# Kernel optimization log

Measured on AMD Instinct MI355X. Metric: run time of the kernel, lower is better.

## Reference

```python
import jax, jax.numpy as jnp
import numpy as np

B, T, D = 2, 1024, 1024
NH, HD = 16, 64          # attention heads, head dim (D = NH*HD)
M = 16                   # LRU block size
H = D // M               # number of LRU blocks = 64
EPS = 1e-5
ROPE_BASE = 10000.0


def rmsnorm(x, w):
    ms = jnp.mean(x * x, axis=-1, keepdims=True)
    return x * jax.lax.rsqrt(ms + EPS) * w


def rope_tables(t_len, dtype):
    inv_freq = 1.0 / (ROPE_BASE ** (jnp.arange(0, HD, 2, dtype=jnp.float32) / HD))
    freqs = jnp.arange(t_len, dtype=jnp.float32)[:, None] * inv_freq[None, :]  # [T, HD/2]
    emb = jnp.concatenate([freqs, freqs], axis=-1)                              # [T, HD]
    return emb.astype(dtype)


def apply_rope(x, emb):
    # x: [B, T, NH, HD]
    cos = jnp.cos(emb)[None, :, None, :]
    sin = jnp.sin(emb)[None, :, None, :]
    x1, x2 = jnp.split(x, 2, axis=-1)
    return x * cos + jnp.concatenate([-x2, x1], axis=-1) * sin


def setup_inputs() -> dict:
    key = jax.random.key(0)
    ks = jax.random.split(key, 7)
    w = lambda k, shape: jax.random.normal(k, shape, dtype=jnp.float32) * 0.02
    return {
        "x": jax.random.normal(ks[0], (B, T, D), dtype=jnp.float32),
        "attn_norm_w": jnp.ones((D,), jnp.float32),
        "w_qkv": w(ks[1], (D, 3 * D)),
        "w_attn_out": w(ks[2], (D, D)),
        "lru_norm_w": jnp.ones((D,), jnp.float32),
        "w_v": w(ks[3], (D, D)),
        "w_a": w(ks[4], (D, H * M * (M + 1))),
        "w_out_proj": w(ks[5], (D, D)),
    }


def reference(x, attn_norm_w, w_qkv, w_attn_out, lru_norm_w, w_v, w_a, w_out_proj):
    # ---- RoPE causal attention block (residual) ----
    h = rmsnorm(x, attn_norm_w)
    qkv = (h @ w_qkv).reshape(B, T, 3, NH, HD)
    q, k, v = qkv[:, :, 0], qkv[:, :, 1], qkv[:, :, 2]
    emb = rope_tables(T, x.dtype)
    q = apply_rope(q, emb)
    k = apply_rope(k, emb)
    scores = jnp.einsum("bthd,bshd->bhts", q, k) / jnp.sqrt(jnp.asarray(HD, x.dtype))
    causal = jnp.tril(jnp.ones((T, T), dtype=bool))
    scores = jnp.where(causal[None, None], scores, jnp.asarray(-1e30, x.dtype))
    attn = jax.nn.softmax(scores, axis=-1)
    o = jnp.einsum("bhts,bshd->bthd", attn, v).reshape(B, T, D)
    x = x + o @ w_attn_out

    # ---- BlockDiagonalLRU block (residual) ----
    h2 = rmsnorm(x, lru_norm_w)
    vv = (h2 @ w_v).reshape(B, T, H, M)
    gates = jax.nn.softmax((h2 @ w_a).reshape(B, T, H, M, M + 1), axis=-1)
    a0 = gates[..., 0]   # [B, T, H, M]
    A = gates[..., 1:]   # [B, T, H, M, M]

    def step(state, inp):
        A_t, a0_t, v_t = inp  # [B,H,M,M], [B,H,M], [B,H,M]
        new = jnp.einsum("bhij,bhj->bhi", A_t, state) + a0_t * v_t
        return new, new

    init = jnp.zeros((B, H, M), x.dtype)
    _, outs = jax.lax.scan(
        step, init,
        (jnp.moveaxis(A, 1, 0), jnp.moveaxis(a0, 1, 0), jnp.moveaxis(vv, 1, 0)),
    )
    h_out = jnp.moveaxis(outs, 0, 1).reshape(B, T, D)
    return x + h_out @ w_out_proj
```

## Files before the change

kernel.cpp:

```cpp
#include <hip/hip_runtime.h>


typedef unsigned short u16;
typedef unsigned int   u32;
typedef __bf16 bf16x8 __attribute__((ext_vector_type(8)));
typedef float  f32x4  __attribute__((ext_vector_type(4)));

#define B_  2
#define T_  1024
#define D_  1024
#define NH_ 16
#define HD_ 64
#define H_  64
#define M_  16

__device__ __forceinline__ float b2f(u16 u) {
    return __uint_as_float(((u32)u) << 16);
}
__device__ __forceinline__ u16 f2b(float f) {
    u32 u = __float_as_uint(f);
    u32 r = (u + 0x7FFFu + ((u >> 16) & 1u)) >> 16;
    return (u16)r;
}
__device__ __forceinline__ float blo(u32 u) { return __uint_as_float(u << 16); }
__device__ __forceinline__ float bhi(u32 u) { return __uint_as_float(u & 0xFFFF0000u); }

__device__ __forceinline__ void stage16(const void* gp, void* lp) {
    typedef __attribute__((address_space(1))) const unsigned int GU;
    typedef __attribute__((address_space(3))) unsigned int LU;
    __builtin_amdgcn_global_load_lds((GU*)gp, (LU*)lp, 16, 0, 0);
}

template<int BM, int BN, int BK, int MODE, bool TRUNCK, bool CAUSAL, int SWZ>
__global__ __launch_bounds__(256) void gemm_bt(
    const u16* __restrict__ A, const u16* __restrict__ Bt,
    void* __restrict__ Cout, void* __restrict__ Cout2, void* __restrict__ Cout3,
    const float* __restrict__ addend,
    int M, int N, int K, long strideA, long strideB, long strideC)
{
    constexpr int MT = BM / 32;
    constexpr int NT = BN / 32;
    constexpr int KCH = BK / 8;
    const int z  = blockIdx.z;
    int bx = blockIdx.x, by = blockIdx.y;
    if (SWZ == 2) {
        int f = by * gridDim.x + bx;
        int xcd = f & 7, k = f >> 3;
        by = k & 15;
        bx = xcd * (gridDim.x >> 3) + (k >> 4);
    }
    const int m0 = by * BM;
    const int n0 = bx * BN;
    if (CAUSAL && n0 > m0 + BM - 1) return;
    const int Keff = TRUNCK ? (K < m0 + BM ? K : m0 + BM) : K;

    const u16* Ab = A  + (size_t)z * (size_t)strideA;
    const u16* Bb = Bt + (size_t)z * (size_t)strideB;

    __shared__ alignas(16) u16 As[BM * BK];
    __shared__ alignas(16) u16 Bs[BN * BK];

    const int tid  = threadIdx.x;
    const int lane = tid & 63, w = tid >> 6;
    const int wr = w >> 1, wc = w & 1;
    const int quad = lane >> 4, l16 = lane & 15;

    f32x4 acc[MT][NT] = {};

    constexpr int AITER = (BM * BK / 8) / 256;
    constexpr int BITER = (BN * BK / 8) / 256;

    for (int k0 = 0; k0 < Keff; k0 += BK) {
        #pragma unroll
        for (int it = 0; it < AITER; ++it) {
            int c = it * 256 + tid;
            int m = c / KCH, kc = c % KCH;
            stage16(Ab + (size_t)(m0 + m) * K + k0 + kc * 8,
                    &As[(it * 256 + w * 64) * 8]);
        }
        #pragma unroll
        for (int it = 0; it < BITER; ++it) {
            int c = it * 256 + tid;
            int n = c / KCH, kc = c % KCH;
            stage16(Bb + (size_t)(n0 + n) * K + k0 + kc * 8,
                    &Bs[(it * 256 + w * 64) * 8]);
        }
        __syncthreads();

        #pragma unroll
        for (int kk = 0; kk < BK; kk += 32) {
            bf16x8 af[MT], bfr[NT];
            #pragma unroll
            for (int mt = 0; mt < MT; ++mt)
                af[mt] = *(const bf16x8*)&As[(wr * (BM / 2) + mt * 16 + l16) * BK + kk + quad * 8];
            #pragma unroll
            for (int nt = 0; nt < NT; ++nt)
                bfr[nt] = *(const bf16x8*)&Bs[(wc * (BN / 2) + nt * 16 + l16) * BK + kk + quad * 8];
            #pragma unroll
            for (int mt = 0; mt < MT; ++mt)
                #pragma unroll
                for (int nt = 0; nt < NT; ++nt)
                    acc[mt][nt] = __builtin_amdgcn_mfma_f32_16x16x32_bf16(
                        af[mt], bfr[nt], acc[mt][nt], 0, 0, 0);
        }
        __syncthreads();
    }

    if (MODE == 6) {
        const int reg = n0 >> 10;
        const int hh  = ((n0 & 1023) >> 6) + wc;
        #pragma unroll
        for (int mt = 0; mt < MT; ++mt) {
            #pragma unroll
            for (int r = 0; r < 4; ++r) {
                int row = m0 + wr * (BM / 2) + mt * 16 + quad * 4 + r;
                int t = row & (T_ - 1), bb = row >> 10;
                size_t obase = ((size_t)(bb * NH_ + hh) * T_ + t) * HD_;
                if (reg == 2) {
                    #pragma unroll
                    for (int nt = 0; nt < 4; ++nt)
                        ((u16*)Cout3)[obase + nt * 16 + l16] = f2b(acc[mt][nt][r]);
                } else {
                    u16* dst = (reg == 0) ? (u16*)Cout : (u16*)Cout2;
                    #pragma unroll
                    for (int nt = 0; nt < 2; ++nt) {
                        int i = nt * 16 + l16;
                        float ang = (float)t * exp2f(-(float)i * 0.41524101186092034f);
                        float sn, cs;
                        sincosf(ang, &sn, &cs);
                        float q1 = acc[mt][nt][r], q2 = acc[mt][nt + 2][r];
                        dst[obase + i]      = f2b(q1 * cs - q2 * sn);
                        dst[obase + i + 32] = f2b(q2 * cs + q1 * sn);
                    }
                }
            }
        }
        return;
    }
    #pragma unroll
    for (int mt = 0; mt < MT; ++mt) {
        #pragma unroll
        for (int nt = 0; nt < NT; ++nt) {
            #pragma unroll
            for (int r = 0; r < 4; ++r) {
                int row = m0 + wr * (BM / 2) + mt * 16 + quad * 4 + r;
                int col = n0 + wc * (BN / 2) + nt * 16 + l16;
                float val = acc[mt][nt][r];
                if (MODE == 0) {
                    if (addend) val += addend[(size_t)row * N + col];
                    ((float*)Cout)[(size_t)z * (size_t)strideC + (size_t)row * N + col] = val;
                } else if (MODE == 1) {
                    ((u16*)Cout)[(size_t)z * (size_t)strideC + (size_t)row * N + col] = f2b(val);
                } else if (MODE == 2) {
                    size_t idx = ((size_t)(z >> 4) * T_ + row) * (size_t)D_ + (z & 15) * HD_ + col;
                    ((u16*)Cout)[idx] = f2b(val);
                } else {
                    const int t  = row & (T_ - 1);
                    const int bb = m0 >> 10;
                    const int cg = (n0 >> 4) + wc * (BN / 32) + nt;
                    if (cg >= 1088) {
                        const int hh = cg - 1088;
                        ((float*)Cout2)[(((size_t)(bb * 64 + hh)) * T_ + t) * 16 + l16] = val;
                    } else {
                        const int hh  = cg / 17;
                        const int rem = cg - hh * 17;
                        ((u16*)Cout)[(((size_t)(bb * 64 + hh)) * T_ + t) * 272 + rem * 16 + l16] = f2b(val);
                    }
                }
            }
        }
    }
}

__global__ __launch_bounds__(256) void rmsnorm_k(
    const float* __restrict__ x, const float* __restrict__ w, u16* __restrict__ out)
{
    const int row = blockIdx.x, tid = threadIdx.x;
    float4 v = ((const float4*)(x + (size_t)row * D_))[tid];
    float ss = v.x * v.x + v.y * v.y + v.z * v.z + v.w * v.w;
    #pragma unroll
    for (int o = 32; o >= 1; o >>= 1) ss += __shfl_xor(ss, o, 64);
    __shared__ float red[4];
    if ((tid & 63) == 0) red[tid >> 6] = ss;
    __syncthreads();
    ss = red[0] + red[1] + red[2] + red[3];
    float scale = rsqrtf(ss * (1.0f / D_) + 1e-5f);
    float4 wv = ((const float4*)w)[tid];
    ushort4 o4;
    o4.x = f2b(v.x * scale * wv.x);
    o4.y = f2b(v.y * scale * wv.y);
    o4.z = f2b(v.z * scale * wv.z);
    o4.w = f2b(v.w * scale * wv.w);
    ((ushort4*)(out + (size_t)row * D_))[tid] = o4;
}

__global__ void convT_all(
    const float* __restrict__ wqkv, const float* __restrict__ wao,
    const float* __restrict__ wv,   const float* __restrict__ wa,
    const float* __restrict__ wop,
    u16* __restrict__ wqkvT, u16* __restrict__ waoT,
    u16* __restrict__ waT,   u16* __restrict__ wopT)
{
    const int x = blockIdx.x;
    const float* in; u16* out; int C, xb;
    if (x < 96)       { in = wqkv; out = wqkvT; C = 3072;  xb = x; }
    else if (x < 128) { in = wao;  out = waoT;  C = 1024;  xb = x - 96; }
    else if (x < 160) { in = wv;   out = waT + (size_t)17408 * 1024; C = 1024; xb = x - 128; }
    else if (x < 704) { in = wa;   out = waT;   C = 17408; xb = x - 160; }
    else              { in = wop;  out = wopT;  C = 1024;  xb = x - 704; }
    constexpr int R = 1024;
    __shared__ float tile[32][33];
    const int c0 = xb * 32, r0 = blockIdx.y * 32;
    const int tx = threadIdx.x, ty = threadIdx.y;
    #pragma unroll
    for (int k = 0; k < 4; ++k)
        tile[ty + 8 * k][tx] = in[(size_t)(r0 + ty + 8 * k) * C + c0 + tx];
    __syncthreads();
    #pragma unroll
    for (int k = 0; k < 4; ++k)
        out[(size_t)(c0 + ty + 8 * k) * R + r0 + tx] = f2b(tile[tx][ty + 8 * k]);
}

__global__ void transpose_bf16_k(const u16* __restrict__ in_, u16* __restrict__ out_, int R, int C)
{
    __shared__ u16 tile[32][33];
    const u16* in = in_ + (size_t)blockIdx.z * R * C;
    u16* out      = out_ + (size_t)blockIdx.z * R * C;
    const int c0 = blockIdx.x * 32, r0 = blockIdx.y * 32;
    const int tx = threadIdx.x, ty = threadIdx.y;
    #pragma unroll
    for (int k = 0; k < 4; ++k)
        tile[ty + 8 * k][tx] = in[(size_t)(r0 + ty + 8 * k) * C + c0 + tx];
    __syncthreads();
    #pragma unroll
    for (int k = 0; k < 4; ++k)
        out[(size_t)(c0 + ty + 8 * k) * R + r0 + tx] = tile[tx][ty + 8 * k];
}

__global__ __launch_bounds__(256) void softmax_causal_k(u16* __restrict__ S)
{
    const int w = threadIdx.x >> 6, lane = threadIdx.x & 63;
    const int z = blockIdx.x * 4 + w;
    const int t = z & (T_ - 1);
    u16* row = S + (size_t)z * T_;
    const int n = t + 1;
    const int kmax = (t & ~63) + 64;
    const int kb = lane * 4;
    float v[4][4];
    float mx = -1e30f;
    #pragma unroll
    for (int it = 0; it < 4; ++it) {
        int k = it * 256 + kb;
        if (k < kmax) {
            uint2 d = *(const uint2*)(row + k);
            v[it][0] = (k + 0 < n) ? blo(d.x) * 0.125f : -1e30f;
            v[it][1] = (k + 1 < n) ? bhi(d.x) * 0.125f : -1e30f;
            v[it][2] = (k + 2 < n) ? blo(d.y) * 0.125f : -1e30f;
            v[it][3] = (k + 3 < n) ? bhi(d.y) * 0.125f : -1e30f;
        } else {
            v[it][0] = v[it][1] = v[it][2] = v[it][3] = -1e30f;
        }
        mx = fmaxf(mx, fmaxf(fmaxf(v[it][0], v[it][1]), fmaxf(v[it][2], v[it][3])));
    }
    #pragma unroll
    for (int o = 32; o >= 1; o >>= 1) mx = fmaxf(mx, __shfl_xor(mx, o, 64));
    float sum = 0.f;
    #pragma unroll
    for (int it = 0; it < 4; ++it)
        #pragma unroll
        for (int j = 0; j < 4; ++j) {
            float e = (v[it][j] > -1e29f) ? __expf(v[it][j] - mx) : 0.f;
            v[it][j] = e;
            sum += e;
        }
    #pragma unroll
    for (int o = 32; o >= 1; o >>= 1) sum += __shfl_xor(sum, o, 64);
    float inv = 1.0f / sum;
    #pragma unroll
    for (int it = 0; it < 4; ++it) {
        int k = it * 256 + kb;
        if (k < kmax) {
            uint2 d;
            d.x = (u32)f2b(v[it][0] * inv) | ((u32)f2b(v[it][1] * inv) << 16);
            d.y = (u32)f2b(v[it][2] * inv) | ((u32)f2b(v[it][3] * inv) << 16);
            *(uint2*)(row + k) = d;
        }
    }
}

__device__ __forceinline__ void scan_prep(u16* glds, float* vlds, int lane)
{
    #pragma unroll
    for (int rnd = 0; rnd < 2; ++rnd) {
        float p[4][17];
        #pragma unroll
        for (int j = 0; j < 4; ++j) {
            int r = rnd * 256 + j * 64 + lane;
            const u16* g = &glds[r * 17];
            float vv[17];
            float mx = -1e30f;
            #pragma unroll
            for (int tt = 0; tt < 17; ++tt) { vv[tt] = b2f(g[tt]); mx = fmaxf(mx, vv[tt]); }
            float s = 0.f;
            #pragma unroll
            for (int tt = 0; tt < 17; ++tt) { vv[tt] = __expf(vv[tt] - mx); s += vv[tt]; }
            float inv = 1.0f / s;
            #pragma unroll
            for (int tt = 0; tt < 17; ++tt) p[j][tt] = vv[tt] * inv;
        }
        __syncthreads();
        #pragma unroll
        for (int j = 0; j < 4; ++j) {
            int r = rnd * 256 + j * 64 + lane;
            uint4 w0, w1;
            w0.x = (u32)f2b(p[j][1])  | ((u32)f2b(p[j][2])  << 16);
            w0.y = (u32)f2b(p[j][3])  | ((u32)f2b(p[j][4])  << 16);
            w0.z = (u32)f2b(p[j][5])  | ((u32)f2b(p[j][6])  << 16);
            w0.w = (u32)f2b(p[j][7])  | ((u32)f2b(p[j][8])  << 16);
            w1.x = (u32)f2b(p[j][9])  | ((u32)f2b(p[j][10]) << 16);
            w1.y = (u32)f2b(p[j][11]) | ((u32)f2b(p[j][12]) << 16);
            w1.z = (u32)f2b(p[j][13]) | ((u32)f2b(p[j][14]) << 16);
            w1.w = (u32)f2b(p[j][15]) | ((u32)f2b(p[j][16]) << 16);
            ((uint4*)glds)[r * 2]     = w0;
            ((uint4*)glds)[r * 2 + 1] = w1;
            vlds[r] *= p[j][0];
        }
        __syncthreads();
    }
}

__global__ __launch_bounds__(64) void scan_p1(
    const u16* __restrict__ gates, const float* __restrict__ vvT,
    float* __restrict__ Pmat, float* __restrict__ evec)
{
    const int c = blockIdx.x, chain = blockIdx.y;
    const int lane = threadIdx.x;
    const int i = lane >> 2, q = lane & 3;
    __shared__ alignas(16) u16   glds[32 * 272];
    __shared__ alignas(16) float vlds[32 * 16];
    __shared__ alignas(16) float Pb[2][256];
    __shared__ float slds[16];

    const char* gbase = (const char*)(gates + ((size_t)chain * T_ + c * 32) * 272);
    #pragma unroll
    for (int it = 0; it < 17; ++it)
        stage16(gbase + it * 1024 + lane * 16, (char*)glds + it * 1024);
    const char* vbase = (const char*)(vvT + ((size_t)chain * T_ + c * 32) * 16);
    #pragma unroll
    for (int it = 0; it < 2; ++it)
        stage16(vbase + it * 1024 + lane * 16, (char*)vlds + it * 1024);
    __syncthreads();

    scan_prep(glds, vlds, lane);

    {
        f32x4 idq;
        #pragma unroll
        for (int m = 0; m < 4; ++m) idq[m] = (i == q * 4 + m) ? 1.f : 0.f;
        *(f32x4*)&Pb[0][i * 16 + q * 4] = idq;
    }
    f32x4 e4[4] = {};
    f32x4 np = {};
    float neLast = 0.f;
    int cur = 0;

    for (int st = 0; st < 32; ++st) {
        const uint4* rp = (const uint4*)((const char*)glds + (st * 16 + i) * 32);
        uint4 d0 = rp[0], d1 = rp[1];
        float ar[16];
        ar[0]  = blo(d0.x); ar[1]  = bhi(d0.x);
        ar[2]  = blo(d0.y); ar[3]  = bhi(d0.y);
        ar[4]  = blo(d0.z); ar[5]  = bhi(d0.z);
        ar[6]  = blo(d0.w); ar[7]  = bhi(d0.w);
        ar[8]  = blo(d1.x); ar[9]  = bhi(d1.x);
        ar[10] = blo(d1.y); ar[11] = bhi(d1.y);
        ar[12] = blo(d1.z); ar[13] = bhi(d1.z);
        ar[14] = blo(d1.w); ar[15] = bhi(d1.w);

        f32x4 pk[16];
        #pragma unroll
        for (int k = 0; k < 16; ++k)
            pk[k] = *(const f32x4*)&Pb[cur][k * 16 + q * 4];

        f32x4 a = pk[0] * ar[0];
        #pragma unroll
        for (int k = 1; k < 16; ++k) a += pk[k] * ar[k];
        np = a;

        float ne0 = ar[0] * e4[0][0] + ar[1] * e4[0][1] + ar[2] * e4[0][2] + ar[3] * e4[0][3];
        float ne1 = ar[4] * e4[1][0] + ar[5] * e4[1][1] + ar[6] * e4[1][2] + ar[7] * e4[1][3];
        float ne2 = ar[8] * e4[2][0] + ar[9] * e4[2][1] + ar[10] * e4[2][2] + ar[11] * e4[2][3];
        float ne3 = ar[12] * e4[3][0] + ar[13] * e4[3][1] + ar[14] * e4[3][2] + ar[15] * e4[3][3];
        float ne = (ne0 + ne1) + (ne2 + ne3) + vlds[st * 16 + i];

        *(f32x4*)&Pb[cur ^ 1][i * 16 + q * 4] = np;
        if (q == 0) slds[i] = ne;
        #pragma unroll
        for (int m = 0; m < 4; ++m) e4[m] = *(const f32x4*)&slds[m * 4];
        neLast = ne;
        cur ^= 1;
    }

    float* Pd = Pmat + ((size_t)chain * 32 + c) * 256;
    *(f32x4*)&Pd[i * 16 + q * 4] = np;
    if (q == 0) evec[((size_t)chain * 32 + c) * 16 + i] = neLast;
}

__global__ __launch_bounds__(64) void scan_comb(
    const float* __restrict__ Pmat, const float* __restrict__ evec, float* __restrict__ sIn)
{
    const int chain = blockIdx.x;
    const int lane = threadIdx.x;
    const int i = lane >> 2, q = lane & 3;
    __shared__ alignas(16) float Pl[32 * 256];
    __shared__ alignas(16) float El[32 * 16];
    __shared__ float slds[16];

    const char* Pg = (const char*)(Pmat + (size_t)chain * 32 * 256);
    #pragma unroll
    for (int it = 0; it < 32; ++it)
        stage16(Pg + it * 1024 + lane * 16, (char*)Pl + it * 1024);
    const char* Eg = (const char*)(evec + (size_t)chain * 32 * 16);
    #pragma unroll
    for (int it = 0; it < 2; ++it)
        stage16(Eg + it * 1024 + lane * 16, (char*)El + it * 1024);
    __syncthreads();

    f32x4 s4[4] = {};
    if (q == 0) sIn[((size_t)chain * 32 + 0) * 16 + i] = 0.f;
    for (int cc = 0; cc < 32; ++cc) {
        f32x4 pr[4];
        #pragma unroll
        for (int m = 0; m < 4; ++m)
            pr[m] = *(const f32x4*)&Pl[cc * 256 + i * 16 + m * 4];
        float ne = 0.f;
        #pragma unroll
        for (int k = 0; k < 16; ++k) ne += pr[k >> 2][k & 3] * s4[k >> 2][k & 3];
        ne += El[cc * 16 + i];
        if (q == 0) {
            slds[i] = ne;
            if (cc < 31) sIn[((size_t)chain * 32 + cc + 1) * 16 + i] = ne;
        }
        #pragma unroll
        for (int m = 0; m < 4; ++m) s4[m] = *(const f32x4*)&slds[m * 4];
    }
}

__global__ __launch_bounds__(64) void scan_p2(
    const u16* __restrict__ gates, const float* __restrict__ vvT,
    const float* __restrict__ sIn, u16* __restrict__ hout)
{
    const int c = blockIdx.x, chain = blockIdx.y;
    const int b = chain >> 6, hh = chain & 63;
    const int lane = threadIdx.x;
    const int i = lane >> 2, q = lane & 3;
    __shared__ alignas(16) u16   glds[32 * 272];
    __shared__ alignas(16) float vlds[32 * 16];
    __shared__ float slds[16];

    const char* gbase = (const char*)(gates + ((size_t)chain * T_ + c * 32) * 272);
    #pragma unroll
    for (int it = 0; it < 17; ++it)
        stage16(gbase + it * 1024 + lane * 16, (char*)glds + it * 1024);
    const char* vbase = (const char*)(vvT + ((size_t)chain * T_ + c * 32) * 16);
    #pragma unroll
    for (int it = 0; it < 2; ++it)
        stage16(vbase + it * 1024 + lane * 16, (char*)vlds + it * 1024);
    __syncthreads();

    scan_prep(glds, vlds, lane);

    const float* sp = sIn + ((size_t)chain * 32 + c) * 16;
    f32x4 s4[4];
    #pragma unroll
    for (int m = 0; m < 4; ++m) s4[m] = *(const f32x4*)(sp + m * 4);

    u16* hbase = hout + ((size_t)(b * T_ + c * 32)) * D_ + hh * 16;
    for (int st = 0; st < 32; ++st) {
        const uint4* rp = (const uint4*)((const char*)glds + (st * 16 + i) * 32);
        uint4 d0 = rp[0], d1 = rp[1];
        float ne0 = blo(d0.x) * s4[0][0] + bhi(d0.x) * s4[0][1]
                  + blo(d0.y) * s4[0][2] + bhi(d0.y) * s4[0][3];
        float ne1 = blo(d0.z) * s4[1][0] + bhi(d0.z) * s4[1][1]
                  + blo(d0.w) * s4[1][2] + bhi(d0.w) * s4[1][3];
        float ne2 = blo(d1.x) * s4[2][0] + bhi(d1.x) * s4[2][1]
                  + blo(d1.y) * s4[2][2] + bhi(d1.y) * s4[2][3];
        float ne3 = blo(d1.z) * s4[3][0] + bhi(d1.z) * s4[3][1]
                  + blo(d1.w) * s4[3][2] + bhi(d1.w) * s4[3][3];
        float ne = (ne0 + ne1) + (ne2 + ne3) + vlds[st * 16 + i];
        if (q == 0) {
            slds[i] = ne;
            hbase[(size_t)st * D_ + i] = f2b(ne);
        }
        #pragma unroll
        for (int m = 0; m < 4; ++m) s4[m] = *(const f32x4*)&slds[m * 4];
    }
}

extern "C" void kernel_launch(void* const* d_in, const int* in_sizes, int n_in,
                              void* d_out, int out_size, void* d_ws, size_t ws_size,
                              hipStream_t stream)
{
    const float* x    = (const float*)d_in[0];
    const float* anw  = (const float*)d_in[1];
    const float* wqkv = (const float*)d_in[2];
    const float* wao  = (const float*)d_in[3];
    const float* lnw  = (const float*)d_in[4];
    const float* wv   = (const float*)d_in[5];
    const float* wa   = (const float*)d_in[6];
    const float* wop  = (const float*)d_in[7];

    char* ws = (char*)d_ws;
    const size_t MB = 1u << 20;
    u16*   h     = (u16*)  (ws +   0 * MB);
    u16*   h2    = (u16*)  (ws +   4 * MB);
    u16*   wqkvT = (u16*)  (ws +   8 * MB);
    u16*   waoT  = (u16*)  (ws +  14 * MB);
    u16*   wopT  = (u16*)  (ws +  16 * MB);
    u16*   waT   = (u16*)  (ws +  18 * MB);
    float* x2    = (float*)(ws +  54 * MB);
    float* vvT   = (float*)(ws +  62 * MB);
    u16*   Qb    = (u16*)  (ws +  78 * MB);
    float* Pmat  = (float*)(ws +  78 * MB);
    u16*   Kb    = (u16*)  (ws +  82 * MB);
    float* evec  = (float*)(ws +  82 * MB);
    float* sIn   = (float*)(ws +  82 * MB + 256 * 1024);
    u16*   Vb    = (u16*)  (ws +  86 * MB);
    u16*   Vt    = (u16*)  (ws +  90 * MB);
    u16*   S     = (u16*)  (ws +  94 * MB);
    u16*   omat  = (u16*)  (ws + 158 * MB);
    u16*   gates = (u16*)  (ws +  94 * MB);
    u16*   hout  = (u16*)  (ws + 162 * MB);
    (void)in_sizes; (void)n_in; (void)out_size; (void)ws_size;

    dim3 tb(32, 8);
    convT_all<<<dim3(736, 32), tb, 0, stream>>>(
        wqkv, wao, wv, wa, wop, wqkvT, waoT, waT, wopT);

    rmsnorm_k<<<2048, 256, 0, stream>>>(x, anw, h);
    gemm_bt<64, 128, 32, 6, false, false, 0><<<dim3(24, 32, 1), 256, 0, stream>>>(
        h, wqkvT, (void*)Qb, (void*)Kb, (void*)Vb, nullptr, 2048, 3072, 1024, 0, 0, 0);
    transpose_bf16_k<<<dim3(2, 32, 32), tb, 0, stream>>>(Vb, Vt, 1024, 64);

    gemm_bt<128, 128, 64, 1, false, true, 0><<<dim3(8, 8, 32), 256, 0, stream>>>(
        Qb, Kb, (void*)S, nullptr, nullptr, nullptr, 1024, 1024, 64, 65536, 65536, 1048576);
    softmax_causal_k<<<8192, 256, 0, stream>>>(S);
    gemm_bt<64, 64, 64, 2, true, false, 0><<<dim3(1, 16, 32), 256, 0, stream>>>(
        S, Vt, (void*)omat, nullptr, nullptr, nullptr, 1024, 64, 1024, 1048576, 65536, 0);

    gemm_bt<64, 128, 32, 0, false, false, 0><<<dim3(8, 32, 1), 256, 0, stream>>>(
        omat, waoT, (void*)x2, nullptr, nullptr, x, 2048, 1024, 1024, 0, 0, 0);
    rmsnorm_k<<<2048, 256, 0, stream>>>(x2, lnw, h2);

    gemm_bt<128, 128, 32, 5, false, false, 2><<<dim3(144, 16, 1), 256, 0, stream>>>(
        h2, waT, (void*)gates, (void*)vvT, nullptr, nullptr, 2048, 18432, 1024, 0, 0, 0);

    scan_p1<<<dim3(32, 128), 64, 0, stream>>>(gates, vvT, Pmat, evec);
    scan_comb<<<128, 64, 0, stream>>>(Pmat, evec, sIn);
    scan_p2<<<dim3(32, 128), 64, 0, stream>>>(gates, vvT, sIn, hout);

    gemm_bt<64, 128, 32, 0, false, false, 0><<<dim3(8, 32, 1), 256, 0, stream>>>(
        hout, wopT, d_out, nullptr, nullptr, x2, 2048, 1024, 1024, 0, 0, 0);
}
```

Baseline: 496.2 us.

## Add dedicated 256x256-tile double-buffered GEMM kernel for LRU gate projection

Replaces the generic 128x128 GEMM used for the large gates/vv projection (2048x18432x1024) with a specialized 512-thread kernel using 256x256 tiles. It adds double-buffered LDS staging with swizzled layout, explicit vmcnt waits and barriers, and s_setprio around the MFMA blocks. Blocks are remapped so neighbours land on the same XCD, aiming at better L2 reuse. The goal is higher arithmetic intensity and better overlap of loads with MFMA on the largest GEMM, at the cost of larger LDS use, lower occupancy and hand-tuned waitcnt logic. It relies on a stage16 helper defined elsewhere in the file.

```diff
diff --git a/kernel.cpp b/kernel.cpp
--- a/kernel.cpp
+++ b/kernel.cpp
@@ -154,17 +154,128 @@
                 } else if (MODE == 2) {
                     size_t idx = ((size_t)(z >> 4) * T_ + row) * (size_t)D_ + (z & 15) * HD_ + col;
                     ((u16*)Cout)[idx] = f2b(val);
-                } else {
-                    const int t  = row & (T_ - 1);
-                    const int bb = m0 >> 10;
-                    const int cg = (n0 >> 4) + wc * (BN / 32) + nt;
+                }
+            }
+        }
+    }
+}
+
+__global__ __launch_bounds__(512) void gemm256_gates(
+    const u16* __restrict__ A, const u16* __restrict__ Bt,
+    u16* __restrict__ gates, float* __restrict__ vvT)
+{
+    constexpr int K = 1024;
+    constexpr int NTILE = 16;
+
+    int f = blockIdx.y * gridDim.x + blockIdx.x;
+    int xcd = f & 7, k = f >> 3;
+    const int by = k & 7;
+    const int bx = xcd * 9 + (k >> 3);
+    const int m0 = by * 256;
+    const int n0 = bx * 256;
+    (void)n0;
+
+    __shared__ alignas(16) u16 sA[2][2][8192];
+    __shared__ alignas(16) u16 sB[2][2][8192];
+
+    const int tid  = threadIdx.x;
+    const int lane = tid & 63, w = tid >> 6;
+    const int wr = w >> 2, wc = w & 3;
+    const int quad = lane >> 4, l16 = lane & 15;
+    const int f2l = (l16 & 3) ^ ((l16 >> 2) & 3);
+    const int sq  = quad ^ f2l;
+
+    const u16* srcA[2];
+    const u16* srcB[2];
+    int ldofs[2];
+    #pragma unroll
+    for (int it = 0; it < 2; ++it) {
+        int sp = it * 512 + tid;
+        int r  = sp >> 2;
+        int sl = (sp & 3) ^ ((r & 3) ^ ((r >> 2) & 3));
+        srcA[it] = A  + (size_t)(m0 + r) * K + sl * 8;
+        srcB[it] = Bt + (size_t)(n0 + r) * K + sl * 8;
+        ldofs[it] = (it * 512 + (tid & ~63)) * 8;
+    }
+
+    const int aoff = (wr * 128 + l16) * 32 + sq * 8;
+    const int boff = (wc * 64  + l16) * 32 + sq * 8;
+
+    f32x4 acc[2][4][4] = {};
+
+#define STG(piece, srcArr, ko)                                     \
+    { stage16(srcArr[0] + (ko), &(piece)[ldofs[0]]);               \
+      stage16(srcArr[1] + (ko), &(piece)[ldofs[1]]); }
+
+#define MFMA_BLK(OM)                                               \
+    __builtin_amdgcn_s_setprio(1);                                 \
+    { _Pragma("unroll") for (int mt = 0; mt < 4; ++mt) {           \
+        _Pragma("unroll") for (int nt = 0; nt < 4; ++nt)           \
+          acc[OM][mt][nt] = __builtin_amdgcn_mfma_f32_16x16x32_bf16(\
+              af[mt], bfr[nt], acc[OM][mt][nt], 0, 0, 0); } }      \
+    __builtin_amdgcn_s_setprio(0);
+
+    STG(sA[0][0], srcA, 0);  STG(sB[0][0], srcB, 0);
+    STG(sA[0][1], srcA, 32); STG(sB[0][1], srcB, 32);
+
+    for (int t = 0; t < NTILE; ++t) {
+        const int cur = t & 1, nxt = cur ^ 1;
+        const int kn = (t < NTILE - 1 ? t + 1 : t) * 64;
+        const u16* Ap0 = sA[cur][0];
+        const u16* Bp0 = sB[cur][0];
+        const u16* Ap1 = sA[cur][1];
+        const u16* Bp1 = sB[cur][1];
+        bf16x8 af[4], bfr[4];
+
+        asm volatile("s_waitcnt vmcnt(4)\n\ts_barrier" ::: "memory");
+
+        #pragma unroll
+        for (int nt = 0; nt < 4; ++nt) bfr[nt] = *(const bf16x8*)&Bp0[boff + nt * 512];
+        #pragma unroll
+        for (int mt = 0; mt < 4; ++mt) af[mt]  = *(const bf16x8*)&Ap0[aoff + mt * 512];
+        STG(sA[nxt][0], srcA, kn);
+        MFMA_BLK(0)
+
+        #pragma unroll
+        for (int mt = 0; mt < 4; ++mt) af[mt]  = *(const bf16x8*)&Ap0[aoff + 2048 + mt * 512];
+        STG(sB[nxt][0], srcB, kn);
+        MFMA_BLK(1)
+
+        asm volatile("s_waitcnt vmcnt(4)\n\ts_barrier" ::: "memory");
+
+        #pragma unroll
+        for (int nt = 0; nt < 4; ++nt) bfr[nt] = *(const bf16x8*)&Bp1[boff + nt * 512];
+        #pragma unroll
+        for (int mt = 0; mt < 4; ++mt) af[mt]  = *(const bf16x8*)&Ap1[aoff + mt * 512];
+        STG(sA[nxt][1], srcA, kn + 32);
+        MFMA_BLK(0)
+
+        #pragma unroll
+        for (int mt = 0; mt < 4; ++mt) af[mt]  = *(const bf16x8*)&Ap1[aoff + 2048 + mt * 512];
+        STG(sB[nxt][1], srcB, kn + 32);
+        MFMA_BLK(1)
+    }
+#undef STG
+#undef MFMA_BLK
+
+    const int cgbase = bx * 16 + wc * 4;
+    #pragma unroll
+    for (int om = 0; om < 2; ++om) {
+        #pragma unroll
+        for (int mt = 0; mt < 4; ++mt) {
+            #pragma unroll
+            for (int r = 0; r < 4; ++r) {
+                int row = m0 + wr * 128 + om * 64 + mt * 16 + quad * 4 + r;
+                int tt = row & (T_ - 1), bb = row >> 10;
+                #pragma unroll
+                for (int nt = 0; nt < 4; ++nt) {
+                    int cg = cgbase + nt;
+                    float val = acc[om][mt][nt][r];
                     if (cg >= 1088) {
-                        const int hh = cg - 1088;
-                        ((float*)Cout2)[(((size_t)(bb * 64 + hh)) * T_ + t) * 16 + l16] = val;
+                        vvT[(((size_t)(bb * 64 + (cg - 1088))) * T_ + tt) * 16 + l16] = val;
                     } else {
-                        const int hh  = cg / 17;
-                        const int rem = cg - hh * 17;
-                        ((u16*)Cout)[(((size_t)(bb * 64 + hh)) * T_ + t) * 272 + rem * 16 + l16] = f2b(val);
+                        int hh = cg / 17, rem = cg - hh * 17;
+                        gates[(((size_t)(bb * 64 + hh)) * T_ + tt) * 272 + rem * 16 + l16] = f2b(val);
                     }
                 }
             }
@@ -552,8 +663,7 @@
         omat, waoT, (void*)x2, nullptr, nullptr, x, 2048, 1024, 1024, 0, 0, 0);
     rmsnorm_k<<<2048, 256, 0, stream>>>(x2, lnw, h2);
 
-    gemm_bt<128, 128, 32, 5, false, false, 2><<<dim3(144, 16, 1), 256, 0, stream>>>(
-        h2, waT, (void*)gates, (void*)vvT, nullptr, nullptr, 2048, 18432, 1024, 0, 0, 0);
+    gemm256_gates<<<dim3(72, 8), 512, 0, stream>>>(h2, waT, gates, vvT);
 
     scan_p1<<<dim3(32, 128), 64, 0, stream>>>(gates, vvT, Pmat, evec);
     scan_comb<<<128, 64, 0, stream>>>(Pmat, evec, sIn);
```

Measured after the change: 512.0 us. 1.03x slower.

## Add dedicated 256x192 pipelined gates GEMM with XCD-aware tile mapping

Applied to the files above, without the earlier changes.

Replaces the generic 128x128 GEMM for the large gates/vv projection (2048x18432x1024) with a specialized 512-thread kernel using 256x192 tiles, double-buffered LDS with XOR swizzle, interleaved staging of the next K-tile between MFMA groups, s_setprio, and a block-to-XCD remapping for L2 locality. The goal is higher MFMA utilization and less global traffic on the dominant GEMM. It adds hand-tuned waitcnt/barrier scheduling, which is fragile and depends on stage16 semantics, and it removes MODE 3 from the generic epilogue.

```diff
diff --git a/kernel.cpp b/kernel.cpp
--- a/kernel.cpp
+++ b/kernel.cpp
@@ -154,17 +154,149 @@
                 } else if (MODE == 2) {
                     size_t idx = ((size_t)(z >> 4) * T_ + row) * (size_t)D_ + (z & 15) * HD_ + col;
                     ((u16*)Cout)[idx] = f2b(val);
-                } else {
-                    const int t  = row & (T_ - 1);
-                    const int bb = m0 >> 10;
-                    const int cg = (n0 >> 4) + wc * (BN / 32) + nt;
+                }
+            }
+        }
+    }
+}
+
+__global__ __launch_bounds__(512, 2) void gemm256_gates(
+    const u16* __restrict__ A, const u16* __restrict__ Bt,
+    u16* __restrict__ gates, float* __restrict__ vvT)
+{
+    constexpr int K = 1024;
+    constexpr int NTILE = 16;
+
+    const int f = blockIdx.y * gridDim.x + blockIdx.x;
+    const int xcd = f & 7, k = f >> 3;
+    const int by = k & 7;
+    const int bx = xcd * 12 + (k >> 3);
+    const int m0 = by * 256;
+    const int n0 = bx * 192;
+
+    __shared__ alignas(16) u16 sA[2][256 * 64];
+    __shared__ alignas(16) u16 sB[2][192 * 64];
+
+    const int tid  = threadIdx.x;
+    const int lane = tid & 63, w = tid >> 6;
+    const int wr = w >> 2, wc = w & 3;
+    const int quad = lane >> 4, l16 = lane & 15;
+
+    const int colOff = (((tid & 7) ^ ((tid >> 3) & 7)) * 8);
+    const u16* pA = A  + (size_t)(m0 + (tid >> 3)) * K + colOff;
+    const u16* pB = Bt + (size_t)(n0 + (tid >> 3)) * K + colOff;
+    const int wbase = (tid >> 6) * 512;
+
+    const int sq0 = quad ^ (l16 & 7);
+    const int sq1 = sq0 ^ 4;
+    const int aoff0 = (wr * 128 + l16) * 64 + sq0 * 8;
+    const int aoff1 = (wr * 128 + l16) * 64 + sq1 * 8;
+    const int boff0 = (wc * 48  + l16) * 64 + sq0 * 8;
+    const int boff1 = (wc * 48  + l16) * 64 + sq1 * 8;
+
+    f32x4 acc[2][4][3] = {};
+
+    u16* sAc = sA[0]; u16* sAn = sA[1];
+    u16* sBc = sB[0]; u16* sBn = sB[1];
+
+    stage16(pB,                    sBc + wbase);
+    stage16(pB + (size_t) 64 * K,  sBc +  4096 + wbase);
+    stage16(pB + (size_t)128 * K,  sBc +  8192 + wbase);
+    stage16(pA,                    sAc + wbase);
+    stage16(pA + (size_t)128 * K,  sAc +  8192 + wbase);
+    stage16(pA + (size_t) 64 * K,  sAc +  4096 + wbase);
+    stage16(pA + (size_t)192 * K,  sAc + 12288 + wbase);
+    asm volatile("s_waitcnt vmcnt(2)" ::: "memory");
+    __builtin_amdgcn_s_barrier();
+
+    bf16x8 af[4], bfr[3];
+
+#define MFMA12(MH)                                                   \
+    __builtin_amdgcn_s_setprio(1);                                   \
+    { _Pragma("unroll") for (int mt = 0; mt < 4; ++mt) {             \
+        _Pragma("unroll") for (int nt = 0; nt < 3; ++nt)             \
+          acc[MH][mt][nt] = __builtin_amdgcn_mfma_f32_16x16x32_bf16( \
+              af[mt], bfr[nt], acc[MH][mt][nt], 0, 0, 0); } }        \
+    __builtin_amdgcn_s_setprio(0);
+
+    #pragma unroll 1
+    for (int t = 0; t < NTILE; ++t) {
+        const size_t kc = (size_t)((t < NTILE - 1 ? t + 1 : t) * 64);
+        bfr[0] = *(const bf16x8*)&sBc[boff0];
+        bfr[1] = *(const bf16x8*)&sBc[boff0 + 1024];
+        bfr[2] = *(const bf16x8*)&sBc[boff0 + 2048];
+        af[0]  = *(const bf16x8*)&sAc[aoff0];
+        af[1]  = *(const bf16x8*)&sAc[aoff0 + 1024];
+        af[2]  = *(const bf16x8*)&sAc[aoff0 + 2048];
+        af[3]  = *(const bf16x8*)&sAc[aoff0 + 3072];
+        stage16(pB + kc,                   sBn + wbase);
+        stage16(pB + (size_t) 64 * K + kc, sBn + 4096 + wbase);
+        stage16(pB + (size_t)128 * K + kc, sBn + 8192 + wbase);
+        __builtin_amdgcn_s_barrier();
+        asm volatile("s_waitcnt lgkmcnt(0)" ::: "memory");
+        MFMA12(0)
+        asm volatile("s_waitcnt vmcnt(3)" ::: "memory");
+        __builtin_amdgcn_s_barrier();
+
+        af[0]  = *(const bf16x8*)&sAc[aoff0 + 4096];
+        af[1]  = *(const bf16x8*)&sAc[aoff0 + 5120];
+        af[2]  = *(const bf16x8*)&sAc[aoff0 + 6144];
+        af[3]  = *(const bf16x8*)&sAc[aoff0 + 7168];
+        stage16(pA + kc,                   sAn + wbase);
+        stage16(pA + (size_t)128 * K + kc, sAn + 8192 + wbase);
+        __builtin_amdgcn_s_barrier();
+        asm volatile("s_waitcnt lgkmcnt(0)" ::: "memory");
+        MFMA12(1)
+        __builtin_amdgcn_s_barrier();
+
+        bfr[0] = *(const bf16x8*)&sBc[boff1];
+        bfr[1] = *(const bf16x8*)&sBc[boff1 + 1024];
+        bfr[2] = *(const bf16x8*)&sBc[boff1 + 2048];
+        af[0]  = *(const bf16x8*)&sAc[aoff1];
+        af[1]  = *(const bf16x8*)&sAc[aoff1 + 1024];
+        af[2]  = *(const bf16x8*)&sAc[aoff1 + 2048];
+        af[3]  = *(const bf16x8*)&sAc[aoff1 + 3072];
+        stage16(pA + (size_t) 64 * K + kc, sAn +  4096 + wbase);
+        stage16(pA + (size_t)192 * K + kc, sAn + 12288 + wbase);
+        __builtin_amdgcn_s_barrier();
+        asm volatile("s_waitcnt lgkmcnt(0)" ::: "memory");
+        MFMA12(0)
+        __builtin_amdgcn_s_barrier();
+
+        af[0]  = *(const bf16x8*)&sAc[aoff1 + 4096];
+        af[1]  = *(const bf16x8*)&sAc[aoff1 + 5120];
+        af[2]  = *(const bf16x8*)&sAc[aoff1 + 6144];
+        af[3]  = *(const bf16x8*)&sAc[aoff1 + 7168];
+        __builtin_amdgcn_s_barrier();
+        asm volatile("s_waitcnt lgkmcnt(0)" ::: "memory");
+        MFMA12(1)
+        asm volatile("s_waitcnt vmcnt(2)" ::: "memory");
+        __builtin_amdgcn_s_barrier();
+
+        u16* tp;
+        tp = sAc; sAc = sAn; sAn = tp;
+        tp = sBc; sBc = sBn; sBn = tp;
+    }
+#undef MFMA12
+
+    const int cgbase = bx * 12 + wc * 3;
+    #pragma unroll
+    for (int mh = 0; mh < 2; ++mh) {
+        #pragma unroll
+        for (int mt = 0; mt < 4; ++mt) {
+            #pragma unroll
+            for (int r = 0; r < 4; ++r) {
+                int row = m0 + wr * 128 + mh * 64 + mt * 16 + quad * 4 + r;
+                int tt = row & (T_ - 1), bb = row >> 10;
+                #pragma unroll
+                for (int nt = 0; nt < 3; ++nt) {
+                    int cg = cgbase + nt;
+                    float val = acc[mh][mt][nt][r];
                     if (cg >= 1088) {
-                        const int hh = cg - 1088;
-                        ((float*)Cout2)[(((size_t)(bb * 64 + hh)) * T_ + t) * 16 + l16] = val;
+                        vvT[(((size_t)(bb * 64 + (cg - 1088))) * T_ + tt) * 16 + l16] = val;
                     } else {
-                        const int hh  = cg / 17;
-                        const int rem = cg - hh * 17;
-                        ((u16*)Cout)[(((size_t)(bb * 64 + hh)) * T_ + t) * 272 + rem * 16 + l16] = f2b(val);
+                        int hh = cg / 17, rem = cg - hh * 17;
+                        gates[(((size_t)(bb * 64 + hh)) * T_ + tt) * 272 + rem * 16 + l16] = f2b(val);
                     }
                 }
             }
@@ -552,8 +684,7 @@
         omat, waoT, (void*)x2, nullptr, nullptr, x, 2048, 1024, 1024, 0, 0, 0);
     rmsnorm_k<<<2048, 256, 0, stream>>>(x2, lnw, h2);
 
-    gemm_bt<128, 128, 32, 5, false, false, 2><<<dim3(144, 16, 1), 256, 0, stream>>>(
-        h2, waT, (void*)gates, (void*)vvT, nullptr, nullptr, 2048, 18432, 1024, 0, 0, 0);
+    gemm256_gates<<<dim3(96, 8), 512, 0, stream>>>(h2, waT, gates, vvT);
 
     scan_p1<<<dim3(32, 128), 64, 0, stream>>>(gates, vvT, Pmat, evec);
     scan_comb<<<128, 64, 0, stream>>>(Pmat, evec, sIn);
```

Measured after the change: 481.1 us. -3.0%, faster.

## Add dedicated 256x288-tile double-buffered GEMM for LRU gate projection

Applied to the files above, without the earlier changes.

Replaces the generic 128x128 gemm_bt for the large gate/value projection (N=18432) with a specialized 512-thread kernel using 256x288 tiles, 64-wide K steps, XOR-swizzled LDS, double buffering and an XCD-aware block remap. Larger tiles raise arithmetic intensity and cut global/L2 traffic for the dominant GEMM, and the 288 width aligns with the 17-column gate groups. The cost is much higher LDS and register use (36 accumulators per lane), which limits occupancy. Mode 3 is dropped from the generic kernel's epilogue.

```diff
diff --git a/kernel.cpp b/kernel.cpp
--- a/kernel.cpp
+++ b/kernel.cpp
@@ -154,18 +154,117 @@
                 } else if (MODE == 2) {
                     size_t idx = ((size_t)(z >> 4) * T_ + row) * (size_t)D_ + (z & 15) * HD_ + col;
                     ((u16*)Cout)[idx] = f2b(val);
+                }
+            }
+        }
+    }
+}
+
+__global__ __launch_bounds__(512, 2) void gemm256_gates(
+    const u16* __restrict__ A, const u16* __restrict__ Bt,
+    u16* __restrict__ gates, float* __restrict__ vvT)
+{
+    constexpr int K = 1024;
+    constexpr int NTILE = 16;
+
+    const int f = blockIdx.y * gridDim.x + blockIdx.x;
+    const int xcd = f & 7, kb_ = f >> 3;
+    const int by = kb_ & 7;
+    const int bx = xcd * 8 + (kb_ >> 3);
+    const int m0 = by * 256;
+    const int n0 = bx * 288;
+
+    __shared__ alignas(16) u16 sA[2][256 * 64];
+    __shared__ alignas(16) u16 sB[2][288 * 64];
+    __shared__ alignas(16) u16 dmp[2048];
+
+    const int tid  = threadIdx.x;
+    const int lane = tid & 63, w = tid >> 6;
+    const int wr = w >> 1, wc = w & 1;
+    const int quad = lane >> 4, l16 = lane & 15;
+
+    const int colOff = (((tid & 7) ^ ((tid >> 3) & 7)) * 8);
+    const u16* pA  = A  + (size_t)(m0 + (tid >> 3)) * K + colOff;
+    const u16* pB  = Bt + (size_t)(n0 + (tid >> 3)) * K + colOff;
+    const u16* pBh = Bt + (size_t)(n0 + 256 + ((tid >> 3) & 31)) * K + colOff;
+    const int wbase = w * 512;
+
+    const int sq0 = quad ^ (l16 & 7);
+    const int sq1 = sq0 ^ 4;
+    const int aoff0 = (wr * 64  + l16) * 64 + sq0 * 8;
+    const int aoff1 = (wr * 64  + l16) * 64 + sq1 * 8;
+    const int boff0 = (wc * 144 + l16) * 64 + sq0 * 8;
+    const int boff1 = (wc * 144 + l16) * 64 + sq1 * 8;
+
+    f32x4 acc[4][9] = {};
+
+    u16* sAc = sA[0]; u16* sAn = sA[1];
+    u16* sBc = sB[0]; u16* sBn = sB[1];
+
+#define STG(dA, dB, kc)                                              \
+    stage16(pA + (kc),                   (dA) + wbase);              \
+    stage16(pA + (size_t) 64 * K + (kc), (dA) +  4096 + wbase);      \
+    stage16(pA + (size_t)128 * K + (kc), (dA) +  8192 + wbase);      \
+    stage16(pA + (size_t)192 * K + (kc), (dA) + 12288 + wbase);      \
+    stage16(pB + (kc),                   (dB) + wbase);              \
+    stage16(pB + (size_t) 64 * K + (kc), (dB) +  4096 + wbase);      \
+    stage16(pB + (size_t)128 * K + (kc), (dB) +  8192 + wbase);      \
+    stage16(pB + (size_t)192 * K + (kc), (dB) + 12288 + wbase);      \
+    stage16(pBh + (kc), (w < 4) ? ((dB) + 16384 + wbase) : (dmp + wbase - 2048));
+
+#define MFMA36                                                       \
+    __builtin_amdgcn_s_setprio(1);                                   \
+    { _Pragma("unroll") for (int mt = 0; mt < 4; ++mt) {             \
+        _Pragma("unroll") for (int nt = 0; nt < 9; ++nt)             \
+          acc[mt][nt] = __builtin_amdgcn_mfma_f32_16x16x32_bf16(     \
+              af[mt], bfr[nt], acc[mt][nt], 0, 0, 0); } }            \
+    __builtin_amdgcn_s_setprio(0);
+
+    STG(sAc, sBc, 0)
+    asm volatile("s_waitcnt vmcnt(0)" ::: "memory");
+    __builtin_amdgcn_s_barrier();
+
+    #pragma unroll 1
+    for (int t = 0; t < NTILE; ++t) {
+        const int kc = (t < NTILE - 1 ? t + 1 : t) * 64;
+        STG(sAn, sBn, kc)
+
+        bf16x8 af[4], bfr[9];
+        #pragma unroll
+        for (int nt = 0; nt < 9; ++nt) bfr[nt] = *(const bf16x8*)&sBc[boff0 + nt * 1024];
+        #pragma unroll
+        for (int mt = 0; mt < 4; ++mt) af[mt]  = *(const bf16x8*)&sAc[aoff0 + mt * 1024];
+        MFMA36
+        #pragma unroll
+        for (int nt = 0; nt < 9; ++nt) bfr[nt] = *(const bf16x8*)&sBc[boff1 + nt * 1024];
+        #pragma unroll
+        for (int mt = 0; mt < 4; ++mt) af[mt]  = *(const bf16x8*)&sAc[aoff1 + mt * 1024];
+        MFMA36
+
+        asm volatile("s_waitcnt vmcnt(0)\n\ts_barrier" ::: "memory");
+        u16* tp;
+        tp = sAc; sAc = sAn; sAn = tp;
+        tp = sBc; sBc = sBn; sBn = tp;
+    }
+#undef STG
+#undef MFMA36
+
+    const int cgbase = bx * 18 + wc * 9;
+    #pragma unroll
+    for (int mt = 0; mt < 4; ++mt) {
+        #pragma unroll
+        for (int r = 0; r < 4; ++r) {
+            int row = m0 + wr * 64 + mt * 16 + quad * 4 + r;
+            int tt = row & (T_ - 1), bb = row >> 10;
+            #pragma unroll
+            for (int nt = 0; nt < 9; ++nt) {
+                int cg = cgbase + nt;
+                float val = acc[mt][nt][r];
+                if (cg >= 1088) {
+                    vvT[(((size_t)(bb * 64 + (cg - 1088))) * T_ + tt) * 16 + l16] = val;
                 } else {
-                    const int t  = row & (T_ - 1);
-                    const int bb = m0 >> 10;
-                    const int cg = (n0 >> 4) + wc * (BN / 32) + nt;
-                    if (cg >= 1088) {
-                        const int hh = cg - 1088;
-                        ((float*)Cout2)[(((size_t)(bb * 64 + hh)) * T_ + t) * 16 + l16] = val;
-                    } else {
-                        const int hh  = cg / 17;
-                        const int rem = cg - hh * 17;
-                        ((u16*)Cout)[(((size_t)(bb * 64 + hh)) * T_ + t) * 272 + rem * 16 + l16] = f2b(val);
-                    }
+                    int hh = cg / 17, rem = cg - hh * 17;
+                    gates[(((size_t)(bb * 64 + hh)) * T_ + tt) * 272 + rem * 16 + l16] = f2b(val);
                 }
             }
         }
@@ -552,8 +651,7 @@
         omat, waoT, (void*)x2, nullptr, nullptr, x, 2048, 1024, 1024, 0, 0, 0);
     rmsnorm_k<<<2048, 256, 0, stream>>>(x2, lnw, h2);
 
-    gemm_bt<128, 128, 32, 5, false, false, 2><<<dim3(144, 16, 1), 256, 0, stream>>>(
-        h2, waT, (void*)gates, (void*)vvT, nullptr, nullptr, 2048, 18432, 1024, 0, 0, 0);
+    gemm256_gates<<<dim3(64, 8), 512, 0, stream>>>(h2, waT, gates, vvT);
 
     scan_p1<<<dim3(32, 128), 64, 0, stream>>>(gates, vvT, Pmat, evec);
     scan_comb<<<128, 64, 0, stream>>>(Pmat, evec, sIn);
```

Measured after the change: 486.1 us. -2.0%, faster.
